# Performance work log

Measured on AMD Instinct MI355X. Metric: run time of the kernel, lower is better.

## Reference

```python
import jax, jax.numpy as jnp
import numpy as np
import math

HEADS = 8

def setup_inputs() -> dict:
    key = jax.random.key(0)
    k1, k2 = jax.random.split(key)
    B, C, H, W = 8, 512, 32, 32
    x = jax.random.normal(k1, (B, C, H, W), dtype=jnp.float32)
    # weight-norm 1x1 conv params: v ~ N(0, 0.05), g initialized to ||v|| (torch weight_norm default)
    proj_v = jax.random.normal(k2, (3 * C, C), dtype=jnp.float32) * 0.05
    proj_g = jnp.linalg.norm(proj_v, axis=1)
    proj_b = jnp.zeros((3 * C,), dtype=jnp.float32)
    return {"x": x, "proj_v": proj_v, "proj_g": proj_g, "proj_b": proj_b}

def reference(x, proj_v, proj_g, proj_b):
    B, C, H, W = x.shape
    heads = HEADS
    dim = C // heads
    N = H * W
    # weight-normalized 1x1 conv: w = g * v / ||v|| per output channel
    w = proj_g[:, None] * proj_v / jnp.linalg.norm(proj_v, axis=1, keepdims=True)
    c = jnp.einsum('oc,bchw->bohw', w, x) + proj_b[None, :, None, None]
    c = c.reshape(B, 3, heads, dim, N)
    q, k, v = c[:, 0], c[:, 1], c[:, 2]  # each (B, heads, dim, N)
    scale = 1.0 / math.sqrt(dim)
    attn = jnp.einsum('bhdq,bhdk->bhqk', q, k) * scale  # (B, heads, N, N)
    attn = jax.nn.softmax(attn, axis=-1)
    out = jnp.einsum('bhdk,bhqk->bhdq', v, attn)  # (B, heads, dim, N)
    return x + out.reshape(B, C, H, W)
```

## Files before the change

kernel.cpp:

```cpp
#include <hip/hip_runtime.h>

typedef _Float16 f16;
typedef _Float16 f16x2 __attribute__((ext_vector_type(2)));
typedef _Float16 f16x4 __attribute__((ext_vector_type(4)));
typedef _Float16 f16x8 __attribute__((ext_vector_type(8)));
typedef float f32x4 __attribute__((ext_vector_type(4)));
typedef float f32x16 __attribute__((ext_vector_type(16)));
typedef unsigned int u32;
typedef unsigned int u32x4 __attribute__((ext_vector_type(4)));

__device__ inline f32x16 mfma32(f16x8 a, f16x8 b, f32x16 c) {
    return __builtin_amdgcn_mfma_f32_32x32x16_f16(a, b, c, 0, 0, 0);
}

__device__ inline u32 pk2u(float a, float b) {
    return __builtin_bit_cast(u32, __builtin_amdgcn_cvt_pkrtz(a, b));
}

__device__ inline void st8(f16* p, f16x8 v) {
    *(f16x4*)p = __builtin_shufflevector(v, v, 0, 1, 2, 3);
    *(f16x4*)(p + 4) = __builtin_shufflevector(v, v, 4, 5, 6, 7);
}
__device__ inline f16x8 ld8(const f16* p) {
    f16x4 lo = *(const f16x4*)p;
    f16x4 hi = *(const f16x4*)(p + 4);
    return __builtin_shufflevector(lo, hi, 0, 1, 2, 3, 4, 5, 6, 7);
}

__global__ __launch_bounds__(256) void prep_k(const float* __restrict__ pv,
                                              const float* __restrict__ pg,
                                              f16* __restrict__ w,
                                              const float* __restrict__ x,
                                              f16* __restrict__ xT) {
    int bid = blockIdx.x;
    if (bid < 1536) {
        int o = bid;
        const float* row = pv + (size_t)o * 512;
        float s = 0.f;
        for (int c = threadIdx.x; c < 512; c += 256) { float t = row[c]; s += t * t; }
        for (int off = 32; off; off >>= 1) s += __shfl_down(s, off, 64);
        __shared__ float red[4];
        int lane = threadIdx.x & 63, wid = threadIdx.x >> 6;
        if (lane == 0) red[wid] = s;
        __syncthreads();
        float tot = red[0] + red[1] + red[2] + red[3];
        float scale = pg[o] * rsqrtf(tot);
        for (int c = threadIdx.x; c < 512; c += 256)
            w[(size_t)o * 512 + c] = (f16)(row[c] * scale);
    } else {
        int t2 = bid - 1536;
        int n0 = (t2 & 31) * 32, c0 = ((t2 >> 5) & 15) * 32, b = t2 >> 9;
        int tx = threadIdx.x & 31, ty = threadIdx.x >> 5;
        __shared__ float t[32][33];
        const float* xb = x + (size_t)b * 512 * 1024;
        for (int i = 0; i < 4; i++)
            t[ty + 8 * i][tx] = xb[(size_t)(c0 + ty + 8 * i) * 1024 + n0 + tx];
        __syncthreads();
        f16* xTb = xT + (size_t)b * 1024 * 512;
        for (int i = 0; i < 4; i++)
            xTb[(size_t)(n0 + ty + 8 * i) * 512 + c0 + tx] = (f16)t[tx][ty + 8 * i];
    }
}

__global__ __launch_bounds__(256) void qkv_gemm_k(const f16* __restrict__ w,
                                                  const f16* __restrict__ xT,
                                                  const float* __restrict__ pb,
                                                  f16* __restrict__ qk,
                                                  f16* __restrict__ v) {
    __shared__ f16 lA[128 * 64];
    __shared__ f16 lB[128 * 64];
    int b = blockIdx.z;
    int oBase = blockIdx.y * 128;
    int nBase = blockIdx.x * 128;
    const f16* xb = xT + (size_t)b * 1024 * 512;
    int tid = threadIdx.x, lane = tid & 63, warp = tid >> 6;
    int wy = warp >> 1, wx = warp & 1;
    int l31 = lane & 31, hi = lane >> 5;

    int srow = lane >> 3;
    int phys = lane & 7;
    int schunk = phys ^ srow;
    const f16* aS[4]; const f16* bS[4]; int ldsOff[4];
    for (int j = 0; j < 4; j++) {
        int rb = (warp * 4 + j) * 8;
        aS[j] = w  + (size_t)(oBase + rb + srow) * 512 + schunk * 8;
        bS[j] = xb + (size_t)(nBase + rb + srow) * 512 + schunk * 8;
        ldsOff[j] = (rb + srow) * 64 + phys * 8;
    }
    int phk[4];
    for (int ks = 0; ks < 4; ks++)
        phk[ks] = (((ks * 2 + hi) ^ (l31 & 7))) * 8;

    f16x8 rA[4], rB[4];
    for (int j = 0; j < 4; j++) {
        rA[j] = *(const f16x8*)aS[j];
        rB[j] = *(const f16x8*)bS[j];
    }

    f32x16 acc[2][2] = {};

    for (int i = 0; i < 8; i++) {
        __syncthreads();
        for (int j = 0; j < 4; j++) {
            *(f16x8*)&lA[ldsOff[j]] = rA[j];
            *(f16x8*)&lB[ldsOff[j]] = rB[j];
        }
        __syncthreads();
        if (i < 7) {
            int k0 = (i + 1) * 64;
            for (int j = 0; j < 4; j++) {
                rA[j] = *(const f16x8*)(aS[j] + k0);
                rB[j] = *(const f16x8*)(bS[j] + k0);
            }
        }
        for (int ks = 0; ks < 4; ks++) {
            f16x8 af[2], bf[2];
            for (int mi = 0; mi < 2; mi++)
                af[mi] = *(f16x8*)&lA[(wy * 64 + mi * 32 + l31) * 64 + phk[ks]];
            for (int ni = 0; ni < 2; ni++)
                bf[ni] = *(f16x8*)&lB[(wx * 64 + ni * 32 + l31) * 64 + phk[ks]];
            for (int mi = 0; mi < 2; mi++)
                for (int ni = 0; ni < 2; ni++)
                    acc[mi][ni] = mfma32(af[mi], bf[ni], acc[mi][ni]);
        }
    }

    int selB = oBase >> 9;
    for (int mi = 0; mi < 2; mi++) {
        for (int g = 0; g < 4; g++) {
            int oR = oBase + wy * 64 + mi * 32 + 8 * g + 4 * hi;
            int h = (oR >> 6) & 7, d0 = oR & 63;
            for (int ni = 0; ni < 2; ni++) {
                int n = nBase + wx * 64 + ni * 32 + l31;
                if (selB < 2) {
                    float sc = selB == 0 ? 0.125f : 1.0f;
                    f16x4 o4;
                    for (int r = 0; r < 4; r++)
                        o4[r] = (f16)((acc[mi][ni][g * 4 + r] + pb[oR + r]) * sc);
                    *(f16x4*)&qk[((((size_t)b * 2 + selB) * 8 + h) * 1024 + n) * 64 + d0] = o4;
                } else {
                    for (int r = 0; r < 4; r++) {
                        float val = acc[mi][ni][g * 4 + r] + pb[oR + r];
                        v[(((size_t)b * 8 + h) * 64 + d0 + r) * 1024 + n] = (f16)val;
                    }
                }
            }
        }
    }
}

#define ALDK 68
__global__ __launch_bounds__(128, 2) void attn_k(const f16* __restrict__ qk,
                                                 const f16* __restrict__ vg,
                                                 const float* __restrict__ x,
                                                 float* __restrict__ out) {
    __shared__ __align__(16) f16 smem[2 * 64 * ALDK];
    f16* lK = smem;
    f16* lV = smem + 64 * ALDK;

    int bh = blockIdx.y;
    int b = bh >> 3, h = bh & 7;
    int qBase = blockIdx.x * 128;
    int tid = threadIdx.x, lane = tid & 63, warp = tid >> 6;
    int l31 = lane & 31, hi = lane >> 5;

    const f16* qbase = qk + (((size_t)b * 2 + 0) * 8 + h) * 1024 * 64;
    const f16* kbase = qk + (((size_t)b * 2 + 1) * 8 + h) * 1024 * 64;
    const f16* vbase = vg + ((size_t)b * 8 + h) * 64 * 1024;

    int q0 = qBase + warp * 64;
    f16x8 aq[2][4];
    for (int qs = 0; qs < 2; qs++)
        for (int ks = 0; ks < 4; ks++)
            aq[qs][ks] = *(const f16x8*)&qbase[(size_t)(q0 + qs * 32 + l31) * 64 + ks * 16 + hi * 8];

    int sr = tid >> 3, sc0 = (tid & 7) * 8;

    f16x8 rK[4], rV[4];
    for (int j = 0; j < 4; j++) {
        rK[j] = *(const f16x8*)&kbase[(size_t)(sr + 16 * j) * 64 + sc0];
        rV[j] = *(const f16x8*)&vbase[(size_t)(sr + 16 * j) * 1024 + sc0];
    }

    f32x16 accO[2][2] = {};
    float l_acc[2] = {0.f, 0.f};

    for (int kt = 0; kt < 16; kt++) {
        __syncthreads();
        for (int j = 0; j < 4; j++) {
            st8(&lK[(sr + 16 * j) * ALDK + sc0], rK[j]);
            st8(&lV[(sr + 16 * j) * ALDK + sc0], rV[j]);
        }
        __syncthreads();
        if (kt < 15) {
            const f16* kb = kbase + (size_t)(kt + 1) * 64 * 64;
            for (int j = 0; j < 4; j++) {
                rK[j] = *(const f16x8*)&kb[(size_t)(sr + 16 * j) * 64 + sc0];
                rV[j] = *(const f16x8*)&vbase[(size_t)(sr + 16 * j) * 1024 + (kt + 1) * 64 + sc0];
            }
        }

        u32 P0[2][2][4], P1[2][2][4];
        float rs[2] = {0.f, 0.f};
        for (int mt = 0; mt < 2; mt++) {
            f16x8 ak[4];
            for (int ks = 0; ks < 4; ks++)
                ak[ks] = ld8(&lK[(mt * 32 + l31) * ALDK + ks * 16 + hi * 8]);
            for (int qs = 0; qs < 2; qs++) {
                f32x16 stt = {};
                for (int ks = 0; ks < 4; ks++)
                    stt = mfma32(ak[ks], aq[qs][ks], stt);
                for (int g = 0; g < 4; g++) {
                    float p0 = __expf(stt[g * 4 + 0]);
                    float p1 = __expf(stt[g * 4 + 1]);
                    float p2 = __expf(stt[g * 4 + 2]);
                    float p3 = __expf(stt[g * 4 + 3]);
                    rs[qs] += (p0 + p1) + (p2 + p3);
                    P0[qs][mt][g] = pk2u(p0, p1);
                    P1[qs][mt][g] = pk2u(p2, p3);
                }
            }
        }
        l_acc[0] += rs[0];
        l_acc[1] += rs[1];

        f16x8 bf[2][4];
        for (int qs = 0; qs < 2; qs++)
            for (int ks = 0; ks < 4; ks++) {
                int mt = ks >> 1, ge = 2 * (ks & 1);
                u32 e00 = P0[qs][mt][ge], e01 = P0[qs][mt][ge + 1];
                u32 e10 = P1[qs][mt][ge], e11 = P1[qs][mt][ge + 1];
                u32 k0 = hi ? e01 : e00;
                u32 k1 = hi ? e11 : e10;
                u32 s0 = hi ? e00 : e01;
                u32 s1 = hi ? e10 : e11;
                u32 r0 = __shfl_xor(s0, 32, 64);
                u32 r1 = __shfl_xor(s1, 32, 64);
                u32 a0 = hi ? r0 : k0, a1 = hi ? r1 : k1;
                u32 b0 = hi ? k0 : r0, b1 = hi ? k1 : r1;
                u32x4 t = {a0, a1, b0, b1};
                bf[qs][ks] = __builtin_bit_cast(f16x8, t);
            }
        for (int dt = 0; dt < 2; dt++) {
            f16x8 av[4];
            for (int ks = 0; ks < 4; ks++)
                av[ks] = ld8(&lV[(dt * 32 + l31) * ALDK + ks * 16 + hi * 8]);
            for (int qs = 0; qs < 2; qs++)
                for (int ks = 0; ks < 4; ks++)
                    accO[qs][dt] = mfma32(av[ks], bf[qs][ks], accO[qs][dt]);
        }
    }

    for (int qs = 0; qs < 2; qs++) {
        float lt = l_acc[qs] + __shfl_xor(l_acc[qs], 32, 64);
        float rl = 1.0f / lt;
        int q = q0 + qs * 32 + l31;
        for (int dt = 0; dt < 2; dt++)
            for (int g = 0; g < 4; g++)
                for (int r = 0; r < 4; r++) {
                    int d = dt * 32 + 8 * g + 4 * hi + r;
                    size_t gi = ((size_t)b * 512 + h * 64 + d) * 1024 + q;
                    out[gi] = x[gi] + accO[qs][dt][g * 4 + r] * rl;
                }
    }
}

extern "C" void kernel_launch(void* const* d_in, const int* in_sizes, int n_in,
                              void* d_out, int out_size, void* d_ws, size_t ws_size,
                              hipStream_t stream) {
    (void)in_sizes; (void)n_in; (void)out_size; (void)ws_size;
    const float* x  = (const float*)d_in[0];
    const float* pv = (const float*)d_in[1];
    const float* pg = (const float*)d_in[2];
    const float* pb = (const float*)d_in[3];
    float* out = (float*)d_out;

    char* ws = (char*)d_ws;
    f16* w   = (f16*)(ws);
    f16* xT  = (f16*)(ws + 1572864);
    f16* qk  = (f16*)(ws + 1572864 + 8388608);
    f16* v   = (f16*)(ws + 1572864 + 8388608 + 16777216);

    hipLaunchKernelGGL(prep_k,     dim3(5632),     dim3(256), 0, stream, pv, pg, w, x, xT);
    hipLaunchKernelGGL(qkv_gemm_k, dim3(8, 12, 8), dim3(256), 0, stream, w, xT, pb, qk, v);
    hipLaunchKernelGGL(attn_k,     dim3(8, 64),    dim3(128), 0, stream, qk, v, x, out);
}
```

Measured before the change: 140.9 us.

## Split attention key range across warp pairs with shared-memory reduction

The attention kernel now uses 256-thread blocks in which two warp groups each process half of the key tiles (0-7 and 8-15) for the same 128 queries. Their partial outputs and row sums are combined through shared memory at the end, and each group writes half of the head dimension. This halves the serial loop length per block and raises the number of waves in flight. The cost is twice the LDS footprint, an extra reduction step, and a swapped grid order so that blocks of the same batch-head are adjacent.

```diff
diff --git a/kernel.cpp b/kernel.cpp
--- a/kernel.cpp
+++ b/kernel.cpp
@@ -150,53 +150,64 @@
 }
 
 #define ALDK 68
-__global__ __launch_bounds__(128, 2) void attn_k(const f16* __restrict__ qk,
+#define HT (64 * ALDK)
+__global__ __launch_bounds__(256, 2) void attn_k(const f16* __restrict__ qk,
                                                  const f16* __restrict__ vg,
                                                  const float* __restrict__ x,
                                                  float* __restrict__ out) {
-    __shared__ __align__(16) f16 smem[2 * 64 * ALDK];
-    f16* lK = smem;
-    f16* lV = smem + 64 * ALDK;
-
-    int bh = blockIdx.y;
+    __shared__ __align__(16) f16 smem[4 * HT];
+    int bh = blockIdx.x;
     int b = bh >> 3, h = bh & 7;
-    int qBase = blockIdx.x * 128;
+    int qBase = blockIdx.y * 128;
     int tid = threadIdx.x, lane = tid & 63, warp = tid >> 6;
+    int wq = warp & 1, wk = warp >> 1;
     int l31 = lane & 31, hi = lane >> 5;
 
     const f16* qbase = qk + (((size_t)b * 2 + 0) * 8 + h) * 1024 * 64;
     const f16* kbase = qk + (((size_t)b * 2 + 1) * 8 + h) * 1024 * 64;
     const f16* vbase = vg + ((size_t)b * 8 + h) * 64 * 1024;
 
-    int q0 = qBase + warp * 64;
+    int q0 = qBase + wq * 64;
     f16x8 aq[2][4];
     for (int qs = 0; qs < 2; qs++)
         for (int ks = 0; ks < 4; ks++)
             aq[qs][ks] = *(const f16x8*)&qbase[(size_t)(q0 + qs * 32 + l31) * 64 + ks * 16 + hi * 8];
 
     int sr = tid >> 3, sc0 = (tid & 7) * 8;
-
-    f16x8 rK[4], rV[4];
-    for (int j = 0; j < 4; j++) {
-        rK[j] = *(const f16x8*)&kbase[(size_t)(sr + 16 * j) * 64 + sc0];
-        rV[j] = *(const f16x8*)&vbase[(size_t)(sr + 16 * j) * 1024 + sc0];
+    f16* myK = smem + wk * 2 * HT;
+    f16* myV = myK + HT;
+
+    f16x8 rg[4][2];
+    for (int j = 0; j < 2; j++) {
+        int r = sr + 32 * j;
+        rg[0][j] = *(const f16x8*)&kbase[(size_t)r * 64 + sc0];
+        rg[1][j] = *(const f16x8*)&vbase[(size_t)r * 1024 + sc0];
+        rg[2][j] = *(const f16x8*)&kbase[(size_t)(8 * 64 + r) * 64 + sc0];
+        rg[3][j] = *(const f16x8*)&vbase[(size_t)r * 1024 + 8 * 64 + sc0];
     }
 
     f32x16 accO[2][2] = {};
     float l_acc[2] = {0.f, 0.f};
 
-    for (int kt = 0; kt < 16; kt++) {
-        __syncthreads();
-        for (int j = 0; j < 4; j++) {
-            st8(&lK[(sr + 16 * j) * ALDK + sc0], rK[j]);
-            st8(&lV[(sr + 16 * j) * ALDK + sc0], rV[j]);
-        }
-        __syncthreads();
-        if (kt < 15) {
-            const f16* kb = kbase + (size_t)(kt + 1) * 64 * 64;
-            for (int j = 0; j < 4; j++) {
-                rK[j] = *(const f16x8*)&kb[(size_t)(sr + 16 * j) * 64 + sc0];
-                rV[j] = *(const f16x8*)&vbase[(size_t)(sr + 16 * j) * 1024 + (kt + 1) * 64 + sc0];
+    for (int i = 0; i < 8; i++) {
+        __syncthreads();
+        for (int j = 0; j < 2; j++) {
+            int r = sr + 32 * j;
+            st8(&smem[0 * HT + r * ALDK + sc0], rg[0][j]);
+            st8(&smem[1 * HT + r * ALDK + sc0], rg[1][j]);
+            st8(&smem[2 * HT + r * ALDK + sc0], rg[2][j]);
+            st8(&smem[3 * HT + r * ALDK + sc0], rg[3][j]);
+        }
+        __syncthreads();
+        if (i < 7) {
+            const f16* kb0 = kbase + (size_t)(i + 1) * 64 * 64;
+            const f16* kb1 = kbase + (size_t)(i + 9) * 64 * 64;
+            for (int j = 0; j < 2; j++) {
+                int r = sr + 32 * j;
+                rg[0][j] = *(const f16x8*)&kb0[(size_t)r * 64 + sc0];
+                rg[1][j] = *(const f16x8*)&vbase[(size_t)r * 1024 + (i + 1) * 64 + sc0];
+                rg[2][j] = *(const f16x8*)&kb1[(size_t)r * 64 + sc0];
+                rg[3][j] = *(const f16x8*)&vbase[(size_t)r * 1024 + (i + 9) * 64 + sc0];
             }
         }
 
@@ -205,7 +216,7 @@
         for (int mt = 0; mt < 2; mt++) {
             f16x8 ak[4];
             for (int ks = 0; ks < 4; ks++)
-                ak[ks] = ld8(&lK[(mt * 32 + l31) * ALDK + ks * 16 + hi * 8]);
+                ak[ks] = ld8(&myK[(mt * 32 + l31) * ALDK + ks * 16 + hi * 8]);
             for (int qs = 0; qs < 2; qs++) {
                 f32x16 stt = {};
                 for (int ks = 0; ks < 4; ks++)
@@ -244,24 +255,48 @@
         for (int dt = 0; dt < 2; dt++) {
             f16x8 av[4];
             for (int ks = 0; ks < 4; ks++)
-                av[ks] = ld8(&lV[(dt * 32 + l31) * ALDK + ks * 16 + hi * 8]);
+                av[ks] = ld8(&myV[(dt * 32 + l31) * ALDK + ks * 16 + hi * 8]);
             for (int qs = 0; qs < 2; qs++)
                 for (int ks = 0; ks < 4; ks++)
                     accO[qs][dt] = mfma32(av[ks], bf[qs][ks], accO[qs][dt]);
         }
     }
 
+    __syncthreads();
+    float* cbuf = (float*)smem;
+    float* pw = cbuf + (size_t)(warp * 64 + lane) * 34;
+    if (wk == 0) {
+        for (int qs = 0; qs < 2; qs++)
+            for (int r = 0; r < 16; r++) pw[qs * 16 + r] = accO[qs][1][r];
+    } else {
+        for (int qs = 0; qs < 2; qs++)
+            for (int r = 0; r < 16; r++) pw[qs * 16 + r] = accO[qs][0][r];
+    }
+    pw[32] = l_acc[0]; pw[33] = l_acc[1];
+    __syncthreads();
+    const float* pr = cbuf + (size_t)((warp ^ 2) * 64 + lane) * 34;
+    float o[2][16];
+    if (wk == 0) {
+        for (int qs = 0; qs < 2; qs++)
+            for (int r = 0; r < 16; r++) o[qs][r] = accO[qs][0][r] + pr[qs * 16 + r];
+    } else {
+        for (int qs = 0; qs < 2; qs++)
+            for (int r = 0; r < 16; r++) o[qs][r] = accO[qs][1][r] + pr[qs * 16 + r];
+    }
+    float lt0 = l_acc[0] + pr[32];
+    float lt1 = l_acc[1] + pr[33];
+
     for (int qs = 0; qs < 2; qs++) {
-        float lt = l_acc[qs] + __shfl_xor(l_acc[qs], 32, 64);
-        float rl = 1.0f / lt;
+        float lts = qs == 0 ? lt0 : lt1;
+        float ltot = lts + __shfl_xor(lts, 32, 64);
+        float rl = 1.0f / ltot;
         int q = q0 + qs * 32 + l31;
-        for (int dt = 0; dt < 2; dt++)
-            for (int g = 0; g < 4; g++)
-                for (int r = 0; r < 4; r++) {
-                    int d = dt * 32 + 8 * g + 4 * hi + r;
-                    size_t gi = ((size_t)b * 512 + h * 64 + d) * 1024 + q;
-                    out[gi] = x[gi] + accO[qs][dt][g * 4 + r] * rl;
-                }
+        for (int g = 0; g < 4; g++)
+            for (int r = 0; r < 4; r++) {
+                int d = wk * 32 + 8 * g + 4 * hi + r;
+                size_t gi = ((size_t)b * 512 + h * 64 + d) * 1024 + q;
+                out[gi] = x[gi] + o[qs][g * 4 + r] * rl;
+            }
     }
 }
 
@@ -283,5 +318,5 @@
 
     hipLaunchKernelGGL(prep_k,     dim3(5632),     dim3(256), 0, stream, pv, pg, w, x, xT);
     hipLaunchKernelGGL(qkv_gemm_k, dim3(8, 12, 8), dim3(256), 0, stream, w, xT, pb, qk, v);
-    hipLaunchKernelGGL(attn_k,     dim3(8, 64),    dim3(128), 0, stream, qk, v, x, out);
-}
+    hipLaunchKernelGGL(attn_k,     dim3(64, 8),    dim3(256), 0, stream, qk, v, x, out);
+}
```

Result: faster. 128.9 us (-8.6%).
